# Kernel optimization log

Hardware: AMD Instinct MI355X
Metric: run time of the kernel (lower is better)

Reference implementation:

```python
import math
import jax, jax.numpy as jnp
import numpy as np

DIM = 1024
N_HEADS = 16
N_KV_HEADS = 4
HEAD_DIM = 64
WINDOW = 512
EPS = 1e-6
B, S = 2, 2048

def _alibi_slopes(n_heads):
    def pow2(n):
        r = 2.0 ** (-8.0 / n)
        return np.array([r ** (i + 1) for i in range(n)], dtype=np.float32)
    if math.log2(n_heads).is_integer():
        return pow2(n_heads)
    m = 2 ** math.floor(math.log2(n_heads))
    return np.concatenate([pow2(m), pow2(2 * m)[::2][: n_heads - m]])

def _rmsnorm(x, w, eps=EPS):
    var = jnp.mean(x * x, axis=-1, keepdims=True)
    return x * jax.lax.rsqrt(var + eps) * w

def setup_inputs() -> dict:
    key = jax.random.key(0)
    ks = jax.random.split(key, 8)
    x = jax.random.normal(ks[0], (B, S, DIM), dtype=jnp.float32)
    wq = 0.02 * jax.random.normal(ks[1], (N_HEADS * HEAD_DIM, DIM), dtype=jnp.float32)
    wk = 0.02 * jax.random.normal(ks[2], (N_KV_HEADS * HEAD_DIM, DIM), dtype=jnp.float32)
    wv = 0.02 * jax.random.normal(ks[3], (N_KV_HEADS * HEAD_DIM, DIM), dtype=jnp.float32)
    wo = 0.02 * jax.random.normal(ks[4], (DIM, N_HEADS * HEAD_DIM), dtype=jnp.float32)
    q_norm_w = jnp.ones((N_HEADS * HEAD_DIM,), dtype=jnp.float32)
    k_norm_w = jnp.ones((N_KV_HEADS * HEAD_DIM,), dtype=jnp.float32)
    return {"x": x, "wq": wq, "wk": wk, "wv": wv, "wo": wo,
            "q_norm_w": q_norm_w, "k_norm_w": k_norm_w}

def reference(x, wq, wk, wv, wo, q_norm_w, k_norm_w):
    bsz, seqlen, _ = x.shape
    repeats = N_HEADS // N_KV_HEADS
    xq = _rmsnorm(x @ wq.T, q_norm_w)
    xk = _rmsnorm(x @ wk.T, k_norm_w)
    xv = x @ wv.T
    # [b, h, s, d]
    q = xq.reshape(bsz, seqlen, N_HEADS, HEAD_DIM).transpose(0, 2, 1, 3)
    k = xk.reshape(bsz, seqlen, N_KV_HEADS, HEAD_DIM).transpose(0, 2, 1, 3)
    v = xv.reshape(bsz, seqlen, N_KV_HEADS, HEAD_DIM).transpose(0, 2, 1, 3)
    k = jnp.repeat(k, repeats, axis=1)
    v = jnp.repeat(v, repeats, axis=1)
    pos = jnp.arange(seqlen)
    rel = pos[None, :] - pos[:, None]  # [s_q, s_k], key - query
    slopes = jnp.asarray(_alibi_slopes(N_HEADS))
    bias = slopes[:, None, None] * rel[None].astype(x.dtype)  # [h, s, s]
    masked = (rel > 0) | (rel < -WINDOW)  # causal + sliding window
    bias = jnp.where(masked[None], -jnp.inf, bias)
    scale = 1.0 / math.sqrt(HEAD_DIM)
    scores = jnp.einsum('bhqd,bhkd->bhqk', q, k) * scale + bias[None]
    probs = jax.nn.softmax(scores, axis=-1)
    y = jnp.einsum('bhqk,bhkd->bhqd', probs, v)
    y = y.transpose(0, 2, 1, 3).reshape(bsz, seqlen, N_HEADS * HEAD_DIM)
    return y @ wo.T
```

## Files before the change

### kernel.cpp

```cpp
#include <hip/hip_runtime.h>

typedef unsigned short u16;
typedef unsigned int u32;

typedef __bf16 bf16x8 __attribute__((ext_vector_type(8)));
typedef float f32x4 __attribute__((ext_vector_type(4)));

__device__ __forceinline__ u16 f2bf(float f) {
  __bf16 h = (__bf16)f;
  return __builtin_bit_cast(u16, h);
}
__device__ __forceinline__ u32 pk2bf(float a, float b) {
  __bf16 lo = (__bf16)a, hi = (__bf16)b;
  return (u32)__builtin_bit_cast(u16, lo) | ((u32)__builtin_bit_cast(u16, hi) << 16);
}
__device__ __forceinline__ float bf2f(u16 v) {
  u32 u = (u32)v << 16;
  return __builtin_bit_cast(float, u);
}

typedef const __attribute__((address_space(1))) u32 gbl_u32;
typedef __attribute__((address_space(3))) u32 lds_u32;
__device__ __forceinline__ void gload_lds16(const u16* g, u16* l) {
  __builtin_amdgcn_global_load_lds((gbl_u32*)g, (lds_u32*)l, 16, 0, 0);
}

__global__ __launch_bounds__(256)
void cvt_all_kernel(const float* __restrict__ x, const float* __restrict__ wq,
                    const float* __restrict__ wk, const float* __restrict__ wv,
                    const float* __restrict__ wo, u16* __restrict__ x_bf,
                    u16* __restrict__ wcat_bf, u16* __restrict__ wo_bf) {
  int t = blockIdx.x * 256 + threadIdx.x;
  const float* src;
  u16* dst;
  if (t < 1048576) {
    src = x; dst = x_bf;
  } else if (t < 1310720) {
    src = wq; dst = wcat_bf; t -= 1048576;
  } else if (t < 1376256) {
    src = wk; dst = wcat_bf + 1048576; t -= 1310720;
  } else if (t < 1441792) {
    src = wv; dst = wcat_bf + 1310720; t -= 1376256;
  } else {
    src = wo; dst = wo_bf; t -= 1441792;
  }
  const int i = t * 4;
  float4 v = *(const float4*)(src + i);
  uint2 p;
  p.x = pk2bf(v.x, v.y);
  p.y = pk2bf(v.z, v.w);
  *(uint2*)(dst + i) = p;
}

template <typename OutT>
__global__ __launch_bounds__(256)
void gemm_bt_kernel(const u16* __restrict__ A, const u16* __restrict__ B,
                    OutT* __restrict__ C, int M, int N, int K) {
  __shared__ u16 As[2][64 * 64];
  __shared__ u16 Bs[2][128 * 64];
  const int tid = threadIdx.x;
  const int lane = tid & 63;
  const int wave = tid >> 6;
  const int wm = (wave >> 1) * 32;
  const int wn = (wave & 1) * 64;
  const int l15 = lane & 15;
  const int quad = lane >> 4;
  const int sw = l15 & 7;
  const size_t bm = (size_t)blockIdx.y * 64;
  const size_t bn = (size_t)blockIdx.x * 128;

  f32x4 acc[2][4];
#pragma unroll
  for (int i = 0; i < 2; ++i)
#pragma unroll
    for (int j = 0; j < 4; ++j) acc[i][j] = f32x4{0.f, 0.f, 0.f, 0.f};

  const int r0 = tid >> 3;
  const int bswz = ((tid & 7) ^ (r0 & 7)) * 8;
  const u16* gA0 = A + (bm + r0) * (size_t)K + bswz;
  const u16* gA1 = A + (bm + r0 + 32) * (size_t)K + bswz;
  const u16* gB0 = B + (bn + r0) * (size_t)K + bswz;
  const u16* gB1 = B + (bn + r0 + 32) * (size_t)K + bswz;
  const u16* gB2 = B + (bn + r0 + 64) * (size_t)K + bswz;
  const u16* gB3 = B + (bn + r0 + 96) * (size_t)K + bswz;

#define FSTAGE(bufi, kk)                                    \
  do {                                                      \
    gload_lds16(gA0 + (kk), &As[bufi][tid * 8]);            \
    gload_lds16(gA1 + (kk), &As[bufi][2048 + tid * 8]);     \
    gload_lds16(gB0 + (kk), &Bs[bufi][tid * 8]);            \
    gload_lds16(gB1 + (kk), &Bs[bufi][2048 + tid * 8]);     \
    gload_lds16(gB2 + (kk), &Bs[bufi][4096 + tid * 8]);     \
    gload_lds16(gB3 + (kk), &Bs[bufi][6144 + tid * 8]);     \
  } while (0)

  FSTAGE(0, 0);
  int buf = 0;
  for (int k0 = 0; k0 < K; k0 += 64) {
    __syncthreads();
    if (k0 + 64 < K) FSTAGE(buf ^ 1, k0 + 64);
    const u16* as = As[buf];
    const u16* bs = Bs[buf];
#pragma unroll
    for (int h = 0; h < 2; ++h) {
      const int cb = quad + 4 * h;
      bf16x8 af[2], bfr[4];
#pragma unroll
      for (int i = 0; i < 2; ++i)
        af[i] = *(const bf16x8*)(&as[(wm + i * 16 + l15) * 64 + ((cb ^ sw) * 8)]);
#pragma unroll
      for (int j = 0; j < 4; ++j)
        bfr[j] = *(const bf16x8*)(&bs[(wn + j * 16 + l15) * 64 + ((cb ^ sw) * 8)]);
#pragma unroll
      for (int i = 0; i < 2; ++i)
#pragma unroll
        for (int j = 0; j < 4; ++j)
          acc[i][j] = __builtin_amdgcn_mfma_f32_16x16x32_bf16(af[i], bfr[j], acc[i][j], 0, 0, 0);
    }
    buf ^= 1;
  }
#undef FSTAGE

  const int rq = quad * 4;
#pragma unroll
  for (int i = 0; i < 2; ++i) {
#pragma unroll
    for (int r = 0; r < 4; ++r) {
      OutT* crow = C + (bm + wm + i * 16 + rq + r) * (size_t)N + bn + wn + l15;
#pragma unroll
      for (int j = 0; j < 4; ++j) {
        if constexpr (sizeof(OutT) == 2)
          crow[j * 16] = f2bf(acc[i][j][r]);
        else
          crow[j * 16] = acc[i][j][r];
      }
    }
  }
}

__global__ __launch_bounds__(256)
void norm_vtrans_kernel(u16* __restrict__ qkv, const float* __restrict__ qw,
                        const float* __restrict__ kw, u16* __restrict__ vt) {
  const int bid = blockIdx.x;
  const int tid = threadIdx.x;
  if (bid < 1024) {
    const int lane = tid & 63, wv = tid >> 6;
    u16* rp = qkv + (size_t)(bid * 4 + wv) * 1536;
    uint4 qa = *(const uint4*)(rp + lane * 16);
    uint4 qb = *(const uint4*)(rp + lane * 16 + 8);
    uint2 kp = *(const uint2*)(rp + 1024 + lane * 4);
    float qv[16];
    const u32* pa = (const u32*)&qa;
    const u32* pb = (const u32*)&qb;
#pragma unroll
    for (int j = 0; j < 4; ++j) {
      qv[2 * j] = bf2f((u16)pa[j]);
      qv[2 * j + 1] = bf2f((u16)(pa[j] >> 16));
      qv[8 + 2 * j] = bf2f((u16)pb[j]);
      qv[9 + 2 * j] = bf2f((u16)(pb[j] >> 16));
    }
    float k0 = bf2f((u16)kp.x), k1 = bf2f((u16)(kp.x >> 16));
    float k2 = bf2f((u16)kp.y), k3 = bf2f((u16)(kp.y >> 16));
    float ss = 0.f;
#pragma unroll
    for (int j = 0; j < 16; ++j) ss = fmaf(qv[j], qv[j], ss);
    float sk = k0 * k0 + k1 * k1 + k2 * k2 + k3 * k3;
#pragma unroll
    for (int off = 1; off < 64; off <<= 1) {
      ss += __shfl_xor(ss, off);
      sk += __shfl_xor(sk, off);
    }
    const float rn = rsqrtf(ss * (1.0f / 1024.0f) + 1e-6f);
    const float rk = rsqrtf(sk * (1.0f / 256.0f) + 1e-6f);
    float4 w0 = *(const float4*)(qw + lane * 16);
    float4 w1 = *(const float4*)(qw + lane * 16 + 4);
    float4 w2 = *(const float4*)(qw + lane * 16 + 8);
    float4 w3 = *(const float4*)(qw + lane * 16 + 12);
    uint4 o1, o2;
    o1.x = pk2bf(qv[0] * rn * w0.x, qv[1] * rn * w0.y);
    o1.y = pk2bf(qv[2] * rn * w0.z, qv[3] * rn * w0.w);
    o1.z = pk2bf(qv[4] * rn * w1.x, qv[5] * rn * w1.y);
    o1.w = pk2bf(qv[6] * rn * w1.z, qv[7] * rn * w1.w);
    o2.x = pk2bf(qv[8] * rn * w2.x, qv[9] * rn * w2.y);
    o2.y = pk2bf(qv[10] * rn * w2.z, qv[11] * rn * w2.w);
    o2.z = pk2bf(qv[12] * rn * w3.x, qv[13] * rn * w3.y);
    o2.w = pk2bf(qv[14] * rn * w3.z, qv[15] * rn * w3.w);
    *(uint4*)(rp + lane * 16) = o1;
    *(uint4*)(rp + lane * 16 + 8) = o2;
    float4 wk4 = *(const float4*)(kw + lane * 4);
    uint2 ko;
    ko.x = pk2bf(k0 * rk * wk4.x, k1 * rk * wk4.y);
    ko.y = pk2bf(k2 * rk * wk4.z, k3 * rk * wk4.w);
    *(uint2*)(rp + 1024 + lane * 4) = ko;
  } else {
    __shared__ u16 shmem[64 * 72];
    const int e = bid - 1024;
    const int t0 = (e & 31) * 64, kvh = (e >> 5) & 3, b = e >> 7;
    u16(*tile)[72] = (u16(*)[72])shmem;
    const int r = tid >> 2, c16 = (tid & 3) * 16;
    const u16* src = qkv + (size_t)(b * 2048 + t0 + r) * 1536 + 1280 + kvh * 64 + c16;
    *(uint4*)&tile[r][c16] = *(const uint4*)src;
    *(uint4*)&tile[r][c16 + 8] = *(const uint4*)(src + 8);
    __syncthreads();
    const int d = tid >> 2, t16 = (tid & 3) * 16;
    u16 o[16];
#pragma unroll
    for (int j = 0; j < 16; ++j) o[j] = tile[t16 + j][d];
    u16* dst = vt + (size_t)((b * 4 + kvh) * 64 + d) * 2048 + t0 + t16;
    *(uint4*)dst = *(uint4*)&o[0];
    *(uint4*)(dst + 8) = *(uint4*)&o[8];
  }
}

__global__ __launch_bounds__(512)
void attn_kernel(const u16* __restrict__ qkvbf, const u16* __restrict__ vt,
                 u16* __restrict__ ybf) {
  __shared__ u16 Ks[2][64 * 64];
  __shared__ u16 Vts[2][64 * 64];
  __shared__ u16 Ps[128 * 72];
  const int qt = blockIdx.x, h = blockIdx.y, b = blockIdx.z;
  const int kvh = h >> 2, q0 = qt * 128;
  const int tid = threadIdx.x, lane = tid & 63, w = tid >> 6;
  const int l15 = lane & 15, quad = lane >> 4;
  const int swl = l15 & 7;

  const u16* qrow = qkvbf + (size_t)(b * 2048 + q0 + w * 16 + l15) * 1536 + h * 64 + quad * 8;
  const bf16x8 qf0 = *(const bf16x8*)qrow;
  const bf16x8 qf1 = *(const bf16x8*)(qrow + 32);

  const int sr = tid >> 3;
  const int bswz = ((tid & 7) ^ (sr & 7)) * 8;
  const u16* kg = qkvbf + (size_t)(b * 2048 + sr) * 1536 + 1024 + kvh * 64 + bswz;
  const u16* vg = vt + (size_t)((b * 4 + kvh) * 64 + sr) * 2048 + bswz;

#define ASTAGE(bufi, cc)                                          \
  do {                                                            \
    gload_lds16(kg + (size_t)(cc) * 1536, &Ks[bufi][tid * 8]);    \
    gload_lds16(vg + (cc), &Vts[bufi][tid * 8]);                  \
  } while (0)

  f32x4 O[4];
#pragma unroll
  for (int jd = 0; jd < 4; ++jd) O[jd] = f32x4{0.f, 0.f, 0.f, 0.f};
  float m_i = -1e30f, l_i = 0.f;
  const float LOG2E = 1.44269504f;
  const float sc2 = 0.125f * LOG2E;
  const float slope2 = exp2f(-0.5f * (float)(h + 1)) * LOG2E;
  const int c_lo = (q0 >= 512) ? (q0 - 512) : 0;
  const int c_hi = q0 + 64;
  const int myq_lo = q0 + w * 16;
  const int myq_hi = myq_lo + 15;
  const int myq = myq_lo + l15;
  const float srr1 = slope2, srr2 = slope2 * 2.0f, srr3 = slope2 * 3.0f;
  const float si16 = slope2 * 16.0f;

  ASTAGE(0, c_lo);
  int buf = 0;

  for (int c = c_lo; c <= c_hi; c += 64) {
    __syncthreads();
    if (c + 64 <= c_hi) ASTAGE(buf ^ 1, c + 64);

    if (!(c > myq_hi || c + 63 < myq_lo - 512)) {
      f32x4 st[4];
      __builtin_amdgcn_s_setprio(1);
#pragma unroll
      for (int i = 0; i < 4; ++i) {
        const int ro = (i * 16 + l15) * 64;
        bf16x8 a0 = *(const bf16x8*)&Ks[buf][ro + ((quad ^ swl) * 8)];
        bf16x8 a1 = *(const bf16x8*)&Ks[buf][ro + (((4 + quad) ^ swl) * 8)];
        f32x4 z = f32x4{0.f, 0.f, 0.f, 0.f};
        z = __builtin_amdgcn_mfma_f32_16x16x32_bf16(a0, qf0, z, 0, 0, 0);
        st[i] = __builtin_amdgcn_mfma_f32_16x16x32_bf16(a1, qf1, z, 0, 0, 0);
      }
      __builtin_amdgcn_s_setprio(0);

      float sv[4][4];
      float rm = -1e30f;
      const bool interior = (c + 63 <= myq_lo) && (c + 512 >= myq_hi);
      if (interior) {
        float bi = slope2 * (float)(c + quad * 4 - myq);
#pragma unroll
        for (int i = 0; i < 4; ++i) {
          float x0 = fmaf(st[i][0], sc2, bi);
          float x1 = fmaf(st[i][1], sc2, bi + srr1);
          float x2 = fmaf(st[i][2], sc2, bi + srr2);
          float x3 = fmaf(st[i][3], sc2, bi + srr3);
          sv[i][0] = x0; sv[i][1] = x1; sv[i][2] = x2; sv[i][3] = x3;
          rm = fmaxf(fmaxf(fmaxf(rm, x0), fmaxf(x1, x2)), x3);
          bi += si16;
        }
      } else {
#pragma unroll
        for (int i = 0; i < 4; ++i)
#pragma unroll
          for (int r = 0; r < 4; ++r) {
            const int key = c + i * 16 + quad * 4 + r;
            const int rel = key - myq;
            float val = (rel > 0 || rel < -512) ? -1e30f
                                                : fmaf(st[i][r], sc2, slope2 * (float)rel);
            sv[i][r] = val;
            rm = fmaxf(rm, val);
          }
      }
      rm = fmaxf(rm, __shfl_xor(rm, 16));
      rm = fmaxf(rm, __shfl_xor(rm, 32));
      const bool nskip = !__all(rm <= m_i + 8.0f);
      float mn = m_i;
      if (nskip) mn = fmaxf(m_i, rm);
      float ls = 0.f;
#pragma unroll
      for (int i = 0; i < 4; ++i) {
        float p0 = exp2f(sv[i][0] - mn);
        float p1 = exp2f(sv[i][1] - mn);
        float p2 = exp2f(sv[i][2] - mn);
        float p3 = exp2f(sv[i][3] - mn);
        ls += (p0 + p1) + (p2 + p3);
        uint2 pw;
        pw.x = pk2bf(p0, p1);
        pw.y = pk2bf(p2, p3);
        *(uint2*)&Ps[(w * 16 + l15) * 72 + i * 16 + quad * 4] = pw;
      }
      ls += __shfl_xor(ls, 16);
      ls += __shfl_xor(ls, 32);
      if (nskip) {
        const float alpha = exp2f(m_i - mn);
        l_i *= alpha;
        m_i = mn;
        float ar[4];
#pragma unroll
        for (int r = 0; r < 4; ++r) ar[r] = __shfl(alpha, quad * 4 + r);
#pragma unroll
        for (int jd = 0; jd < 4; ++jd)
#pragma unroll
          for (int r = 0; r < 4; ++r) O[jd][r] *= ar[r];
      }
      l_i += ls;

      bf16x8 pf0 = *(const bf16x8*)&Ps[(w * 16 + l15) * 72 + quad * 8];
      bf16x8 pf1 = *(const bf16x8*)&Ps[(w * 16 + l15) * 72 + 32 + quad * 8];
      __builtin_amdgcn_s_setprio(1);
#pragma unroll
      for (int jd = 0; jd < 4; ++jd) {
        const int ro = (jd * 16 + l15) * 64;
        bf16x8 v0 = *(const bf16x8*)&Vts[buf][ro + ((quad ^ swl) * 8)];
        bf16x8 v1 = *(const bf16x8*)&Vts[buf][ro + (((4 + quad) ^ swl) * 8)];
        O[jd] = __builtin_amdgcn_mfma_f32_16x16x32_bf16(pf0, v0, O[jd], 0, 0, 0);
        O[jd] = __builtin_amdgcn_mfma_f32_16x16x32_bf16(pf1, v1, O[jd], 0, 0, 0);
      }
      __builtin_amdgcn_s_setprio(0);
    }
    buf ^= 1;
  }
#undef ASTAGE

  float lr[4];
#pragma unroll
  for (int r = 0; r < 4; ++r) lr[r] = __shfl(l_i, quad * 4 + r);
#pragma unroll
  for (int r = 0; r < 4; ++r) {
    const float inv = 1.0f / lr[r];
    u16* orow = ybf + (size_t)(b * 2048 + q0 + w * 16 + quad * 4 + r) * 1024 + h * 64 + l15;
#pragma unroll
    for (int jd = 0; jd < 4; ++jd) orow[jd * 16] = f2bf(O[jd][r] * inv);
  }
}

extern "C" void kernel_launch(void* const* d_in, const int* in_sizes, int n_in,
                              void* d_out, int out_size, void* d_ws, size_t ws_size,
                              hipStream_t stream) {
  const float* x = (const float*)d_in[0];
  const float* wq = (const float*)d_in[1];
  const float* wk = (const float*)d_in[2];
  const float* wv = (const float*)d_in[3];
  const float* wo = (const float*)d_in[4];
  const float* qnw = (const float*)d_in[5];
  const float* knw = (const float*)d_in[6];
  float* out = (float*)d_out;
  char* ws = (char*)d_ws;

  u16* x_bf = (u16*)(ws);
  u16* wcat_bf = (u16*)(ws + 8388608);
  u16* wo_bf = (u16*)(ws + 11534336);
  u16* qkv_bf = (u16*)(ws + 13631488);
  u16* vt_bf = (u16*)(ws + 26214400);
  u16* y_bf = (u16*)(ws + 28311552);

  cvt_all_kernel<<<6656, 256, 0, stream>>>(x, wq, wk, wv, wo, x_bf, wcat_bf, wo_bf);

  gemm_bt_kernel<u16><<<dim3(12, 64), 256, 0, stream>>>(x_bf, wcat_bf, qkv_bf, 4096, 1536, 1024);
  norm_vtrans_kernel<<<1280, 256, 0, stream>>>(qkv_bf, qnw, knw, vt_bf);
  attn_kernel<<<dim3(16, 16, 2), 512, 0, stream>>>(qkv_bf, vt_bf, y_bf);
  gemm_bt_kernel<float><<<dim3(8, 64), 256, 0, stream>>>(y_bf, wo_bf, out, 4096, 1024, 1024);
}
```

Measured before the change: 154.3 us.

## Process two query heads per attention block to reuse staged K/V tiles

Each attention block now handles two query heads that share the same KV head. Every K/V tile staged into LDS is consumed twice, which halves the global-to-LDS traffic and the number of blocks launched (256 instead of 512). The cost is twice the accumulator registers per thread, which may lower occupancy. The shared P scratch buffer is reused back to back by both heads within a wave.

```diff
diff --git a/kernel.cpp b/kernel.cpp
--- a/kernel.cpp
+++ b/kernel.cpp
@@ -212,21 +212,123 @@
   }
 }
 
+__device__ __forceinline__ void attn_head_tile(
+    const u16* __restrict__ Ksb, const u16* __restrict__ Vtsb,
+    u16* __restrict__ Ps, const bf16x8 qf0, const bf16x8 qf1,
+    const float slope2, f32x4 (&O)[4], float& m_i, float& l_i,
+    const int c, const int myq, const int myq_lo, const int myq_hi,
+    const int w, const int l15, const int quad, const int swl) {
+  const float sc2 = 0.125f * 1.44269504f;
+  const float srr1 = slope2, srr2 = slope2 * 2.0f, srr3 = slope2 * 3.0f;
+  const float si16 = slope2 * 16.0f;
+
+  f32x4 st[4];
+  __builtin_amdgcn_s_setprio(1);
+#pragma unroll
+  for (int i = 0; i < 4; ++i) {
+    const int ro = (i * 16 + l15) * 64;
+    bf16x8 a0 = *(const bf16x8*)&Ksb[ro + ((quad ^ swl) * 8)];
+    bf16x8 a1 = *(const bf16x8*)&Ksb[ro + (((4 + quad) ^ swl) * 8)];
+    f32x4 z = f32x4{0.f, 0.f, 0.f, 0.f};
+    z = __builtin_amdgcn_mfma_f32_16x16x32_bf16(a0, qf0, z, 0, 0, 0);
+    st[i] = __builtin_amdgcn_mfma_f32_16x16x32_bf16(a1, qf1, z, 0, 0, 0);
+  }
+  __builtin_amdgcn_s_setprio(0);
+
+  float sv[4][4];
+  float rm = -1e30f;
+  const bool interior = (c + 63 <= myq_lo) && (c + 512 >= myq_hi);
+  if (interior) {
+    float bi = slope2 * (float)(c + quad * 4 - myq);
+#pragma unroll
+    for (int i = 0; i < 4; ++i) {
+      float x0 = fmaf(st[i][0], sc2, bi);
+      float x1 = fmaf(st[i][1], sc2, bi + srr1);
+      float x2 = fmaf(st[i][2], sc2, bi + srr2);
+      float x3 = fmaf(st[i][3], sc2, bi + srr3);
+      sv[i][0] = x0; sv[i][1] = x1; sv[i][2] = x2; sv[i][3] = x3;
+      rm = fmaxf(fmaxf(fmaxf(rm, x0), fmaxf(x1, x2)), x3);
+      bi += si16;
+    }
+  } else {
+#pragma unroll
+    for (int i = 0; i < 4; ++i)
+#pragma unroll
+      for (int r = 0; r < 4; ++r) {
+        const int key = c + i * 16 + quad * 4 + r;
+        const int rel = key - myq;
+        float val = (rel > 0 || rel < -512) ? -1e30f
+                                            : fmaf(st[i][r], sc2, slope2 * (float)rel);
+        sv[i][r] = val;
+        rm = fmaxf(rm, val);
+      }
+  }
+  rm = fmaxf(rm, __shfl_xor(rm, 16));
+  rm = fmaxf(rm, __shfl_xor(rm, 32));
+  const bool nskip = !__all(rm <= m_i + 8.0f);
+  float mn = m_i;
+  if (nskip) mn = fmaxf(m_i, rm);
+  float ls = 0.f;
+#pragma unroll
+  for (int i = 0; i < 4; ++i) {
+    float p0 = exp2f(sv[i][0] - mn);
+    float p1 = exp2f(sv[i][1] - mn);
+    float p2 = exp2f(sv[i][2] - mn);
+    float p3 = exp2f(sv[i][3] - mn);
+    ls += (p0 + p1) + (p2 + p3);
+    uint2 pw;
+    pw.x = pk2bf(p0, p1);
+    pw.y = pk2bf(p2, p3);
+    *(uint2*)&Ps[(w * 16 + l15) * 72 + i * 16 + quad * 4] = pw;
+  }
+  ls += __shfl_xor(ls, 16);
+  ls += __shfl_xor(ls, 32);
+  if (nskip) {
+    const float alpha = exp2f(m_i - mn);
+    l_i *= alpha;
+    m_i = mn;
+    float ar[4];
+#pragma unroll
+    for (int r = 0; r < 4; ++r) ar[r] = __shfl(alpha, quad * 4 + r);
+#pragma unroll
+    for (int jd = 0; jd < 4; ++jd)
+#pragma unroll
+      for (int r = 0; r < 4; ++r) O[jd][r] *= ar[r];
+  }
+  l_i += ls;
+
+  bf16x8 pf0 = *(const bf16x8*)&Ps[(w * 16 + l15) * 72 + quad * 8];
+  bf16x8 pf1 = *(const bf16x8*)&Ps[(w * 16 + l15) * 72 + 32 + quad * 8];
+  __builtin_amdgcn_s_setprio(1);
+#pragma unroll
+  for (int jd = 0; jd < 4; ++jd) {
+    const int ro = (jd * 16 + l15) * 64;
+    bf16x8 v0 = *(const bf16x8*)&Vtsb[ro + ((quad ^ swl) * 8)];
+    bf16x8 v1 = *(const bf16x8*)&Vtsb[ro + (((4 + quad) ^ swl) * 8)];
+    O[jd] = __builtin_amdgcn_mfma_f32_16x16x32_bf16(pf0, v0, O[jd], 0, 0, 0);
+    O[jd] = __builtin_amdgcn_mfma_f32_16x16x32_bf16(pf1, v1, O[jd], 0, 0, 0);
+  }
+  __builtin_amdgcn_s_setprio(0);
+}
+
 __global__ __launch_bounds__(512)
 void attn_kernel(const u16* __restrict__ qkvbf, const u16* __restrict__ vt,
                  u16* __restrict__ ybf) {
   __shared__ u16 Ks[2][64 * 64];
   __shared__ u16 Vts[2][64 * 64];
   __shared__ u16 Ps[128 * 72];
-  const int qt = blockIdx.x, h = blockIdx.y, b = blockIdx.z;
-  const int kvh = h >> 2, q0 = qt * 128;
+  const int qt = blockIdx.x, hp = blockIdx.y, b = blockIdx.z;
+  const int h0 = hp * 2, h1 = h0 + 1;
+  const int kvh = h0 >> 2, q0 = qt * 128;
   const int tid = threadIdx.x, lane = tid & 63, w = tid >> 6;
   const int l15 = lane & 15, quad = lane >> 4;
   const int swl = l15 & 7;
 
-  const u16* qrow = qkvbf + (size_t)(b * 2048 + q0 + w * 16 + l15) * 1536 + h * 64 + quad * 8;
-  const bf16x8 qf0 = *(const bf16x8*)qrow;
-  const bf16x8 qf1 = *(const bf16x8*)(qrow + 32);
+  const u16* qbase = qkvbf + (size_t)(b * 2048 + q0 + w * 16 + l15) * 1536 + quad * 8;
+  const bf16x8 qa0 = *(const bf16x8*)(qbase + h0 * 64);
+  const bf16x8 qa1 = *(const bf16x8*)(qbase + h0 * 64 + 32);
+  const bf16x8 qb0 = *(const bf16x8*)(qbase + h1 * 64);
+  const bf16x8 qb1 = *(const bf16x8*)(qbase + h1 * 64 + 32);
 
   const int sr = tid >> 3;
   const int bswz = ((tid & 7) ^ (sr & 7)) * 8;
@@ -239,20 +341,21 @@
     gload_lds16(vg + (cc), &Vts[bufi][tid * 8]);                  \
   } while (0)
 
-  f32x4 O[4];
-#pragma unroll
-  for (int jd = 0; jd < 4; ++jd) O[jd] = f32x4{0.f, 0.f, 0.f, 0.f};
-  float m_i = -1e30f, l_i = 0.f;
+  f32x4 Oa[4], Ob[4];
+#pragma unroll
+  for (int jd = 0; jd < 4; ++jd) {
+    Oa[jd] = f32x4{0.f, 0.f, 0.f, 0.f};
+    Ob[jd] = f32x4{0.f, 0.f, 0.f, 0.f};
+  }
+  float ma = -1e30f, la = 0.f, mb = -1e30f, lb = 0.f;
   const float LOG2E = 1.44269504f;
-  const float sc2 = 0.125f * LOG2E;
-  const float slope2 = exp2f(-0.5f * (float)(h + 1)) * LOG2E;
+  const float slope_a = exp2f(-0.5f * (float)(h0 + 1)) * LOG2E;
+  const float slope_b = exp2f(-0.5f * (float)(h1 + 1)) * LOG2E;
   const int c_lo = (q0 >= 512) ? (q0 - 512) : 0;
   const int c_hi = q0 + 64;
   const int myq_lo = q0 + w * 16;
   const int myq_hi = myq_lo + 15;
   const int myq = myq_lo + l15;
-  const float srr1 = slope2, srr2 = slope2 * 2.0f, srr3 = slope2 * 3.0f;
-  const float si16 = slope2 * 16.0f;
 
   ASTAGE(0, c_lo);
   int buf = 0;
@@ -262,107 +365,31 @@
     if (c + 64 <= c_hi) ASTAGE(buf ^ 1, c + 64);
 
     if (!(c > myq_hi || c + 63 < myq_lo - 512)) {
-      f32x4 st[4];
-      __builtin_amdgcn_s_setprio(1);
-#pragma unroll
-      for (int i = 0; i < 4; ++i) {
-        const int ro = (i * 16 + l15) * 64;
-        bf16x8 a0 = *(const bf16x8*)&Ks[buf][ro + ((quad ^ swl) * 8)];
-        bf16x8 a1 = *(const bf16x8*)&Ks[buf][ro + (((4 + quad) ^ swl) * 8)];
-        f32x4 z = f32x4{0.f, 0.f, 0.f, 0.f};
-        z = __builtin_amdgcn_mfma_f32_16x16x32_bf16(a0, qf0, z, 0, 0, 0);
-        st[i] = __builtin_amdgcn_mfma_f32_16x16x32_bf16(a1, qf1, z, 0, 0, 0);
-      }
-      __builtin_amdgcn_s_setprio(0);
-
-      float sv[4][4];
-      float rm = -1e30f;
-      const bool interior = (c + 63 <= myq_lo) && (c + 512 >= myq_hi);
-      if (interior) {
-        float bi = slope2 * (float)(c + quad * 4 - myq);
-#pragma unroll
-        for (int i = 0; i < 4; ++i) {
-          float x0 = fmaf(st[i][0], sc2, bi);
-          float x1 = fmaf(st[i][1], sc2, bi + srr1);
-          float x2 = fmaf(st[i][2], sc2, bi + srr2);
-          float x3 = fmaf(st[i][3], sc2, bi + srr3);
-          sv[i][0] = x0; sv[i][1] = x1; sv[i][2] = x2; sv[i][3] = x3;
-          rm = fmaxf(fmaxf(fmaxf(rm, x0), fmaxf(x1, x2)), x3);
-          bi += si16;
-        }
-      } else {
-#pragma unroll
-        for (int i = 0; i < 4; ++i)
-#pragma unroll
-          for (int r = 0; r < 4; ++r) {
-            const int key = c + i * 16 + quad * 4 + r;
-            const int rel = key - myq;
-            float val = (rel > 0 || rel < -512) ? -1e30f
-                                                : fmaf(st[i][r], sc2, slope2 * (float)rel);
-            sv[i][r] = val;
-            rm = fmaxf(rm, val);
-          }
-      }
-      rm = fmaxf(rm, __shfl_xor(rm, 16));
-      rm = fmaxf(rm, __shfl_xor(rm, 32));
-      const bool nskip = !__all(rm <= m_i + 8.0f);
-      float mn = m_i;
-      if (nskip) mn = fmaxf(m_i, rm);
-      float ls = 0.f;
-#pragma unroll
-      for (int i = 0; i < 4; ++i) {
-        float p0 = exp2f(sv[i][0] - mn);
-        float p1 = exp2f(sv[i][1] - mn);
-        float p2 = exp2f(sv[i][2] - mn);
-        float p3 = exp2f(sv[i][3] - mn);
-        ls += (p0 + p1) + (p2 + p3);
-        uint2 pw;
-        pw.x = pk2bf(p0, p1);
-        pw.y = pk2bf(p2, p3);
-        *(uint2*)&Ps[(w * 16 + l15) * 72 + i * 16 + quad * 4] = pw;
-      }
-      ls += __shfl_xor(ls, 16);
-      ls += __shfl_xor(ls, 32);
-      if (nskip) {
-        const float alpha = exp2f(m_i - mn);
-        l_i *= alpha;
-        m_i = mn;
-        float ar[4];
-#pragma unroll
-        for (int r = 0; r < 4; ++r) ar[r] = __shfl(alpha, quad * 4 + r);
-#pragma unroll
-        for (int jd = 0; jd < 4; ++jd)
-#pragma unroll
-          for (int r = 0; r < 4; ++r) O[jd][r] *= ar[r];
-      }
-      l_i += ls;
-
-      bf16x8 pf0 = *(const bf16x8*)&Ps[(w * 16 + l15) * 72 + quad * 8];
-      bf16x8 pf1 = *(const bf16x8*)&Ps[(w * 16 + l15) * 72 + 32 + quad * 8];
-      __builtin_amdgcn_s_setprio(1);
-#pragma unroll
-      for (int jd = 0; jd < 4; ++jd) {
-        const int ro = (jd * 16 + l15) * 64;
-        bf16x8 v0 = *(const bf16x8*)&Vts[buf][ro + ((quad ^ swl) * 8)];
-        bf16x8 v1 = *(const bf16x8*)&Vts[buf][ro + (((4 + quad) ^ swl) * 8)];
-        O[jd] = __builtin_amdgcn_mfma_f32_16x16x32_bf16(pf0, v0, O[jd], 0, 0, 0);
-        O[jd] = __builtin_amdgcn_mfma_f32_16x16x32_bf16(pf1, v1, O[jd], 0, 0, 0);
-      }
-      __builtin_amdgcn_s_setprio(0);
+      attn_head_tile(Ks[buf], Vts[buf], Ps, qa0, qa1, slope_a, Oa, ma, la,
+                     c, myq, myq_lo, myq_hi, w, l15, quad, swl);
+      attn_head_tile(Ks[buf], Vts[buf], Ps, qb0, qb1, slope_b, Ob, mb, lb,
+                     c, myq, myq_lo, myq_hi, w, l15, quad, swl);
     }
     buf ^= 1;
   }
 #undef ASTAGE
 
-  float lr[4];
-#pragma unroll
-  for (int r = 0; r < 4; ++r) lr[r] = __shfl(l_i, quad * 4 + r);
+  float lra[4], lrb[4];
 #pragma unroll
   for (int r = 0; r < 4; ++r) {
-    const float inv = 1.0f / lr[r];
-    u16* orow = ybf + (size_t)(b * 2048 + q0 + w * 16 + quad * 4 + r) * 1024 + h * 64 + l15;
-#pragma unroll
-    for (int jd = 0; jd < 4; ++jd) orow[jd * 16] = f2bf(O[jd][r] * inv);
+    lra[r] = __shfl(la, quad * 4 + r);
+    lrb[r] = __shfl(lb, quad * 4 + r);
+  }
+#pragma unroll
+  for (int r = 0; r < 4; ++r) {
+    const float inva = 1.0f / lra[r];
+    const float invb = 1.0f / lrb[r];
+    u16* orow = ybf + (size_t)(b * 2048 + q0 + w * 16 + quad * 4 + r) * 1024 + l15;
+#pragma unroll
+    for (int jd = 0; jd < 4; ++jd) {
+      orow[h0 * 64 + jd * 16] = f2bf(Oa[jd][r] * inva);
+      orow[h1 * 64 + jd * 16] = f2bf(Ob[jd][r] * invb);
+    }
   }
 }
 
@@ -390,6 +417,6 @@
 
   gemm_bt_kernel<u16><<<dim3(12, 64), 256, 0, stream>>>(x_bf, wcat_bf, qkv_bf, 4096, 1536, 1024);
   norm_vtrans_kernel<<<1280, 256, 0, stream>>>(qkv_bf, qnw, knw, vt_bf);
-  attn_kernel<<<dim3(16, 16, 2), 512, 0, stream>>>(qkv_bf, vt_bf, y_bf);
+  attn_kernel<<<dim3(16, 8, 2), 512, 0, stream>>>(qkv_bf, vt_bf, y_bf);
   gemm_bt_kernel<float><<<dim3(8, 64), 256, 0, stream>>>(y_bf, wo_bf, out, 4096, 1024, 1024);
 }
```

Measured after the change: 158.9 us. +2.9%, slower.
